# Kernel tuning notes

Hardware: AMD Instinct MI355X
Metric: run time of the kernel (lower is better)

The kernel has to match this reference:

```python
import jax, jax.numpy as jnp
import numpy as np

C_IN = 512
C = 64        # per-head dim
N_HEAD = 8
B, S = 2, 2048


def setup_inputs() -> dict:
    key = jax.random.key(0)
    ks = jax.random.split(key, 9)
    scale = 1.0 / np.sqrt(C_IN)
    return {
        "x": jax.random.normal(ks[0], (B, S, C_IN), dtype=jnp.float32),
        "bias": jax.random.normal(ks[1], (B, N_HEAD, S, S), dtype=jnp.float32),
        "Wq": jax.random.normal(ks[2], (N_HEAD * C, C_IN), dtype=jnp.float32) * scale,
        "Wk": jax.random.normal(ks[3], (N_HEAD * C, C_IN), dtype=jnp.float32) * scale,
        "Wv": jax.random.normal(ks[4], (N_HEAD * C, C_IN), dtype=jnp.float32) * scale,
        "Wo": jax.random.normal(ks[5], (C_IN, N_HEAD * C), dtype=jnp.float32) * scale,
        "bo": jax.random.normal(ks[6], (C_IN,), dtype=jnp.float32) * 0.01,
        "Wg": jax.random.normal(ks[7], (N_HEAD * C, C_IN), dtype=jnp.float32) * scale,
        "bg": jax.random.normal(ks[8], (N_HEAD * C,), dtype=jnp.float32) * 0.01,
    }


def reference(x, bias, Wq, Wk, Wv, Wo, bo, Wg, bg):
    # x: [B, S, C_IN]; attn_dim=1 -> q/k/v axis is already at -2 after movedim.
    # Project and split heads: [B, S, H*C] -> [B, H, S, C]
    def split_heads(t):
        Bq, Sq, _ = t.shape
        return t.reshape(Bq, Sq, N_HEAD, C).transpose(0, 2, 1, 3)

    q = split_heads(x @ Wq.T) / jnp.sqrt(jnp.asarray(C, x.dtype))
    k = split_heads(x @ Wk.T)
    v = split_heads(x @ Wv.T)

    a = jnp.einsum("bhqc,bhkc->bhqk", q, k) + bias   # [B, H, S, S]
    a = jax.nn.softmax(a, axis=-1)
    o = jnp.einsum("bhqk,bhkc->bhqc", a, v)          # [B, H, S, C]

    # merge heads back: [B, S, H*C]
    o = o.transpose(0, 2, 1, 3).reshape(x.shape[0], x.shape[1], N_HEAD * C)
    g = jax.nn.sigmoid(x @ Wg.T + bg)
    o = g * o
    return o @ Wo.T + bo                              # [B, S, C_IN]
```

## Files before the change

kernel.cpp:

```cpp
#include <hip/hip_runtime.h>
#include <math.h>

#define BB 2
#define HH 8
#define SS 2048
#define CC 64
#define CIN 512
#define DDIM 512
#define MM (BB*SS)
#define NCHUNK (SS / 64)

#define LOG2E 1.4426950408889634f
#define SHIFT2 (16.0f * LOG2E)

using short8  = __attribute__((ext_vector_type(8))) short;
using float4v = __attribute__((ext_vector_type(4))) float;

__device__ __forceinline__ unsigned short tob(float f) {
    unsigned u = __float_as_uint(f);
    unsigned r = (u + 0x7fffu + ((u >> 16) & 1u)) >> 16;
    return (unsigned short)r;
}
__device__ __forceinline__ float fromb(unsigned short u) {
    return __uint_as_float(((unsigned)u) << 16);
}

__device__ __forceinline__ void barrier_lds_only() {
    __builtin_amdgcn_sched_barrier(0);
    asm volatile("s_waitcnt lgkmcnt(0)" ::: "memory");
    __builtin_amdgcn_s_barrier();
    __builtin_amdgcn_sched_barrier(0);
}

__global__ __launch_bounds__(256) void convert_all(
    const float* __restrict__ x,
    const float* __restrict__ wq, const float* __restrict__ wk,
    const float* __restrict__ wv, const float* __restrict__ wg,
    const float* __restrict__ wo,
    unsigned short* __restrict__ xb,
    unsigned short* __restrict__ wqb, unsigned short* __restrict__ wkb,
    unsigned short* __restrict__ wvb, unsigned short* __restrict__ wgb,
    unsigned short* __restrict__ wob)
{
    const int NX4 = MM * CIN / 4;
    int i = blockIdx.x * blockDim.x + threadIdx.x;
    const float* src; unsigned short* dst; float scale = 1.0f; int off;
    if (i < NX4) { src = x; dst = xb; off = i; }
    else {
        int j = i - NX4;
        int seg = j >> 16;
        off = j & 65535;
        if      (seg == 0) { src = wq; dst = wqb; scale = 0.125f * LOG2E; }
        else if (seg == 1) { src = wk; dst = wkb; }
        else if (seg == 2) { src = wv; dst = wvb; }
        else if (seg == 3) { src = wg; dst = wgb; }
        else               { src = wo; dst = wob; }
    }
    float4 v = ((const float4*)src)[off];
    ushort4 o;
    o.x = tob(v.x * scale); o.y = tob(v.y * scale);
    o.z = tob(v.z * scale); o.w = tob(v.w * scale);
    ((ushort4*)dst)[off] = o;
}

__global__ __launch_bounds__(256) void proj_gemm(
    const unsigned short* __restrict__ X,
    const unsigned short* __restrict__ Wq,
    const unsigned short* __restrict__ Wk,
    const unsigned short* __restrict__ Wv,
    const unsigned short* __restrict__ Wg,
    const float* __restrict__ bg,
    unsigned short* __restrict__ Qd,
    unsigned short* __restrict__ Kd,
    unsigned short* __restrict__ Vd,
    unsigned short* __restrict__ Gd)
{
    __shared__ __align__(16) unsigned short At[64][72];
    __shared__ __align__(16) unsigned short Bt[64][72];

    int mode = blockIdx.z;
    const unsigned short* W = (mode == 0) ? Wq : (mode == 1) ? Wk : (mode == 2) ? Wv : Wg;

    int m0 = blockIdx.y * 64;
    int n0 = blockIdx.x * 64;
    int tid = threadIdx.x;
    int w = tid >> 6, lane = tid & 63;
    int quad = lane >> 4, l16 = lane & 15;
    int wm = w & 1, wn = w >> 1;

    float4v acc[2][2];
    for (int a = 0; a < 2; ++a) for (int c = 0; c < 2; ++c) acc[a][c] = (float4v)0.0f;

    for (int kc = 0; kc < CIN; kc += 64) {
        for (int it = 0; it < 2; ++it) {
            int idx = it * 2048 + tid * 8;
            int row = idx >> 6, col = idx & 63;
            *(short8*)&At[row][col] = *(const short8*)&X[(size_t)(m0 + row) * CIN + kc + col];
            *(short8*)&Bt[row][col] = *(const short8*)&W[(size_t)(n0 + row) * CIN + kc + col];
        }
        __syncthreads();
        for (int ks = 0; ks < 2; ++ks) {
            short8 a0 = *(const short8*)&At[wm * 32 + l16][ks * 32 + quad * 8];
            short8 a1 = *(const short8*)&At[wm * 32 + 16 + l16][ks * 32 + quad * 8];
            short8 b0 = *(const short8*)&Bt[wn * 32 + l16][ks * 32 + quad * 8];
            short8 b1 = *(const short8*)&Bt[wn * 32 + 16 + l16][ks * 32 + quad * 8];
            acc[0][0] = __builtin_amdgcn_mfma_f32_16x16x32_bf16(a0, b0, acc[0][0], 0, 0, 0);
            acc[0][1] = __builtin_amdgcn_mfma_f32_16x16x32_bf16(a0, b1, acc[0][1], 0, 0, 0);
            acc[1][0] = __builtin_amdgcn_mfma_f32_16x16x32_bf16(a1, b0, acc[1][0], 0, 0, 0);
            acc[1][1] = __builtin_amdgcn_mfma_f32_16x16x32_bf16(a1, b1, acc[1][1], 0, 0, 0);
        }
        __syncthreads();
    }

    if (mode == 2) {
        for (int a = 0; a < 2; ++a) for (int c = 0; c < 2; ++c)
            for (int r = 0; r < 4; ++r) {
                int ml = wm * 32 + a * 16 + quad * 4 + r;
                int nl = wn * 32 + c * 16 + l16;
                At[nl][ml] = tob(acc[a][c][r]);
            }
        __syncthreads();
        int bi = m0 >> 11, h = n0 >> 6, s0 = m0 & 2047;
        int crow = tid >> 2, seg = tid & 3;
        unsigned short* dp = Vd + (((size_t)(bi * HH + h) * CC) + crow) * SS + s0 + seg * 16;
        *(short8*)dp       = *(const short8*)&At[crow][seg * 16];
        *(short8*)(dp + 8) = *(const short8*)&At[crow][seg * 16 + 8];
        return;
    }

    for (int a = 0; a < 2; ++a) for (int c = 0; c < 2; ++c)
        for (int r = 0; r < 4; ++r) {
            int gm = m0 + wm * 32 + a * 16 + quad * 4 + r;
            int gn = n0 + wn * 32 + c * 16 + l16;
            float v = acc[a][c][r];
            if (mode <= 1) {
                int bi = gm >> 11, s = gm & 2047, h = gn >> 6, cc = gn & 63;
                unsigned short* d = (mode == 0) ? Qd : Kd;
                d[(((size_t)(bi * HH + h) * SS) + s) * CC + cc] = tob(v);
            } else {
                float g = 1.0f / (1.0f + __expf(-(v + bg[gn])));
                Gd[(size_t)gm * DDIM + gn] = tob(g);
            }
        }
}

__global__ __launch_bounds__(256, 2) void attn_kernel(
    const unsigned short* __restrict__ Q,
    const unsigned short* __restrict__ K,
    const unsigned short* __restrict__ V,
    const float* __restrict__ bias,
    const unsigned short* __restrict__ G,
    unsigned short* __restrict__ Om)
{
    __shared__ __align__(16) unsigned short Kt[64][72];
    __shared__ __align__(16) unsigned short Vt[64][72];
    __shared__ __align__(16) unsigned short Pt[4][16][72];
    __shared__ __align__(16) float Bs[64][68];

    int qb = blockIdx.x * 64;
    int bh = blockIdx.y;
    int b = bh >> 3, h = bh & 7;
    int tid = threadIdx.x;
    int w = tid >> 6, lane = tid & 63;
    int quad = lane >> 4, l16 = lane & 15;

    int phase = (blockIdx.x + blockIdx.y) & (NCHUNK - 1);

    const unsigned short* Qbh = Q + (size_t)bh * SS * CC;
    const unsigned short* Kbh = K + (size_t)bh * SS * CC;
    const unsigned short* Vbh = V + (size_t)bh * CC * SS;
    const float* Bbh = bias + (size_t)bh * SS * SS;

    int qrow = qb + w * 16 + l16;
    short8 aq0 = *(const short8*)&Qbh[(size_t)qrow * CC + quad * 8];
    short8 aq1 = *(const short8*)&Qbh[(size_t)qrow * CC + 32 + quad * 8];

    float lsum[4] = {0.f, 0.f, 0.f, 0.f};
    float4v accO[4];
    for (int jn = 0; jn < 4; ++jn) accO[jn] = (float4v)0.0f;

    int srow0 = (tid * 8) >> 6,        scol0 = (tid * 8) & 63;
    int srow1 = (2048 + tid * 8) >> 6, scol1 = (2048 + tid * 8) & 63;
    int btrow = tid >> 4;
    int btcol = (tid & 15) * 4;

    short8 pk0, pk1, pv0, pv1;
    float4 pb[4];
    {
        int kb0 = phase * 64;
        pk0 = *(const short8*)&Kbh[(size_t)(kb0 + srow0) * CC + scol0];
        pk1 = *(const short8*)&Kbh[(size_t)(kb0 + srow1) * CC + scol1];
        pv0 = *(const short8*)&Vbh[(size_t)srow0 * SS + kb0 + scol0];
        pv1 = *(const short8*)&Vbh[(size_t)srow1 * SS + kb0 + scol1];
#pragma unroll
        for (int rr = 0; rr < 4; ++rr)
            pb[rr] = *(const float4*)&Bbh[(size_t)(qb + rr * 16 + btrow) * SS + kb0 + btcol];
    }

    for (int c = 0; c < NCHUNK; ++c) {
        barrier_lds_only();
        *(short8*)&Kt[srow0][scol0] = pk0;
        *(short8*)&Kt[srow1][scol1] = pk1;
        *(short8*)&Vt[srow0][scol0] = pv0;
        *(short8*)&Vt[srow1][scol1] = pv1;
#pragma unroll
        for (int rr = 0; rr < 4; ++rr)
            *(float4*)&Bs[rr * 16 + btrow][btcol] = pb[rr];

        if (c + 1 < NCHUNK) {
            int kbn = ((c + 1 + phase) & (NCHUNK - 1)) * 64;
            pk0 = *(const short8*)&Kbh[(size_t)(kbn + srow0) * CC + scol0];
            pk1 = *(const short8*)&Kbh[(size_t)(kbn + srow1) * CC + scol1];
            pv0 = *(const short8*)&Vbh[(size_t)srow0 * SS + kbn + scol0];
            pv1 = *(const short8*)&Vbh[(size_t)srow1 * SS + kbn + scol1];
#pragma unroll
            for (int rr = 0; rr < 4; ++rr)
                pb[rr] = *(const float4*)&Bbh[(size_t)(qb + rr * 16 + btrow) * SS + kbn + btcol];
        }

        barrier_lds_only();

        float4v sa[4];
#pragma unroll
        for (int j = 0; j < 4; ++j) sa[j] = (float4v)(-SHIFT2);
#pragma unroll
        for (int j = 0; j < 4; ++j) {
            short8 bk0 = *(const short8*)&Kt[j * 16 + l16][quad * 8];
            short8 bk1 = *(const short8*)&Kt[j * 16 + l16][32 + quad * 8];
            sa[j] = __builtin_amdgcn_mfma_f32_16x16x32_bf16(aq0, bk0, sa[j], 0, 0, 0);
            sa[j] = __builtin_amdgcn_mfma_f32_16x16x32_bf16(aq1, bk1, sa[j], 0, 0, 0);
        }

#pragma unroll
        for (int j = 0; j < 4; ++j)
#pragma unroll
            for (int r = 0; r < 4; ++r) {
                float bb = Bs[w * 16 + quad * 4 + r][j * 16 + l16];
                float p = __builtin_amdgcn_exp2f(fmaf(bb, LOG2E, sa[j][r]));
                lsum[r] += p;
                Pt[w][quad * 4 + r][j * 16 + l16] = tob(p);
            }

#pragma unroll
        for (int ks = 0; ks < 2; ++ks) {
            short8 ap = *(const short8*)&Pt[w][l16][ks * 32 + quad * 8];
#pragma unroll
            for (int jn = 0; jn < 4; ++jn) {
                short8 bv = *(const short8*)&Vt[jn * 16 + l16][ks * 32 + quad * 8];
                accO[jn] = __builtin_amdgcn_mfma_f32_16x16x32_bf16(ap, bv, accO[jn], 0, 0, 0);
            }
        }
    }

    float rl[4];
#pragma unroll
    for (int r = 0; r < 4; ++r) {
        float s = lsum[r];
        s += __shfl_xor(s, 1, 64);
        s += __shfl_xor(s, 2, 64);
        s += __shfl_xor(s, 4, 64);
        s += __shfl_xor(s, 8, 64);
        rl[r] = 1.0f / s;
    }

    int mrow = b * SS + qb + w * 16 + quad * 4;
#pragma unroll
    for (int jn = 0; jn < 4; ++jn)
#pragma unroll
        for (int r = 0; r < 4; ++r) {
            int col = h * 64 + jn * 16 + l16;
            float g = fromb(G[(size_t)(mrow + r) * DDIM + col]);
            Om[(size_t)(mrow + r) * DDIM + col] = tob(accO[jn][r] * rl[r] * g);
        }
}

__global__ __launch_bounds__(256) void out_gemm(
    const unsigned short* __restrict__ Og,
    const unsigned short* __restrict__ W,
    const float* __restrict__ bo,
    float* __restrict__ out)
{
    __shared__ __align__(16) unsigned short At[64][72];
    __shared__ __align__(16) unsigned short Bt[64][72];

    int m0 = blockIdx.y * 64;
    int n0 = blockIdx.x * 64;
    int tid = threadIdx.x;
    int w = tid >> 6, lane = tid & 63;
    int quad = lane >> 4, l16 = lane & 15;
    int wm = w & 1, wn = w >> 1;

    float4v acc[2][2];
    for (int a = 0; a < 2; ++a) for (int c = 0; c < 2; ++c) acc[a][c] = (float4v)0.0f;

    for (int kc = 0; kc < DDIM; kc += 64) {
        for (int it = 0; it < 2; ++it) {
            int idx = it * 2048 + tid * 8;
            int row = idx >> 6, col = idx & 63;
            *(short8*)&At[row][col] = *(const short8*)&Og[(size_t)(m0 + row) * DDIM + kc + col];
            *(short8*)&Bt[row][col] = *(const short8*)&W[(size_t)(n0 + row) * DDIM + kc + col];
        }
        __syncthreads();
        for (int ks = 0; ks < 2; ++ks) {
            short8 a0 = *(const short8*)&At[wm * 32 + l16][ks * 32 + quad * 8];
            short8 a1 = *(const short8*)&At[wm * 32 + 16 + l16][ks * 32 + quad * 8];
            short8 b0 = *(const short8*)&Bt[wn * 32 + l16][ks * 32 + quad * 8];
            short8 b1 = *(const short8*)&Bt[wn * 32 + 16 + l16][ks * 32 + quad * 8];
            acc[0][0] = __builtin_amdgcn_mfma_f32_16x16x32_bf16(a0, b0, acc[0][0], 0, 0, 0);
            acc[0][1] = __builtin_amdgcn_mfma_f32_16x16x32_bf16(a0, b1, acc[0][1], 0, 0, 0);
            acc[1][0] = __builtin_amdgcn_mfma_f32_16x16x32_bf16(a1, b0, acc[1][0], 0, 0, 0);
            acc[1][1] = __builtin_amdgcn_mfma_f32_16x16x32_bf16(a1, b1, acc[1][1], 0, 0, 0);
        }
        __syncthreads();
    }

    for (int a = 0; a < 2; ++a) for (int c = 0; c < 2; ++c)
        for (int r = 0; r < 4; ++r) {
            int gm = m0 + wm * 32 + a * 16 + quad * 4 + r;
            int gn = n0 + wn * 32 + c * 16 + l16;
            out[(size_t)gm * DDIM + gn] = acc[a][c][r] + bo[gn];
        }
}

extern "C" void kernel_launch(void* const* d_in, const int* in_sizes, int n_in,
                              void* d_out, int out_size, void* d_ws, size_t ws_size,
                              hipStream_t stream)
{
    const float* x    = (const float*)d_in[0];
    const float* bias = (const float*)d_in[1];
    const float* Wq   = (const float*)d_in[2];
    const float* Wk   = (const float*)d_in[3];
    const float* Wv   = (const float*)d_in[4];
    const float* Wo   = (const float*)d_in[5];
    const float* bo   = (const float*)d_in[6];
    const float* Wg   = (const float*)d_in[7];
    const float* bg   = (const float*)d_in[8];
    float* out = (float*)d_out;

    char* ws = (char*)d_ws;
    auto alloc = [&](size_t bytes) { char* p = ws; ws += (bytes + 255) & ~(size_t)255; return p; };
    unsigned short* xb  = (unsigned short*)alloc((size_t)MM * CIN * 2);
    unsigned short* wqb = (unsigned short*)alloc((size_t)DDIM * CIN * 2);
    unsigned short* wkb = (unsigned short*)alloc((size_t)DDIM * CIN * 2);
    unsigned short* wvb = (unsigned short*)alloc((size_t)DDIM * CIN * 2);
    unsigned short* wgb = (unsigned short*)alloc((size_t)DDIM * CIN * 2);
    unsigned short* wob = (unsigned short*)alloc((size_t)DDIM * CIN * 2);
    unsigned short* Qh  = (unsigned short*)alloc((size_t)BB * HH * SS * CC * 2);
    unsigned short* Kh  = (unsigned short*)alloc((size_t)BB * HH * SS * CC * 2);
    unsigned short* Vh  = (unsigned short*)alloc((size_t)BB * HH * SS * CC * 2);
    unsigned short* Gt  = (unsigned short*)alloc((size_t)MM * DDIM * 2);
    unsigned short* Om  = (unsigned short*)alloc((size_t)MM * DDIM * 2);

    convert_all<<<3328, 256, 0, stream>>>(x, Wq, Wk, Wv, Wg, Wo,
                                          xb, wqb, wkb, wvb, wgb, wob);
    proj_gemm<<<dim3(DDIM / 64, MM / 64, 4), 256, 0, stream>>>(
        xb, wqb, wkb, wvb, wgb, bg, Qh, Kh, Vh, Gt);
    attn_kernel<<<dim3(SS / 64, BB * HH), 256, 0, stream>>>(
        Qh, Kh, Vh, bias, Gt, Om);
    out_gemm<<<dim3(DDIM / 64, MM / 64), 256, 0, stream>>>(Om, wob, bo, out);
}
```

Before: 493.0 us.

## Stage K/V/bias tiles via direct global-to-LDS loads with double buffering

Replaces register-staged prefetch of K, V and bias tiles with global_load_lds transfers straight into double-buffered LDS, issuing the load two chunks ahead and synchronizing with vmcnt waits. K and V tiles drop the row padding and use an XOR swizzle on 16-byte columns to avoid bank conflicts. The aim is to free VGPRs, remove the LDS store instructions and overlap memory traffic with compute. The cost is more LDS (the bias buffer doubles), which may limit occupancy, and fragile hand-written waitcnt counts.

```diff
diff --git a/kernel.cpp b/kernel.cpp
--- a/kernel.cpp
+++ b/kernel.cpp
@@ -25,12 +25,10 @@
     return __uint_as_float(((unsigned)u) << 16);
 }
 
-__device__ __forceinline__ void barrier_lds_only() {
-    __builtin_amdgcn_sched_barrier(0);
-    asm volatile("s_waitcnt lgkmcnt(0)" ::: "memory");
-    __builtin_amdgcn_s_barrier();
-    __builtin_amdgcn_sched_barrier(0);
-}
+#define GLDS(srcp, ldsp)                                                     \
+    __builtin_amdgcn_global_load_lds(                                        \
+        (const __attribute__((address_space(1))) void*)(srcp),               \
+        (__attribute__((address_space(3))) void*)(ldsp), 16, 0, 0)
 
 __global__ __launch_bounds__(256) void convert_all(
     const float* __restrict__ x,
@@ -152,10 +150,10 @@
     const unsigned short* __restrict__ G,
     unsigned short* __restrict__ Om)
 {
-    __shared__ __align__(16) unsigned short Kt[64][72];
-    __shared__ __align__(16) unsigned short Vt[64][72];
+    __shared__ __align__(16) unsigned short Kt[2][64][64];
+    __shared__ __align__(16) unsigned short Vt[2][64][64];
+    __shared__ __align__(16) float Bs[2][64][64];
     __shared__ __align__(16) unsigned short Pt[4][16][72];
-    __shared__ __align__(16) float Bs[64][68];
 
     int qb = blockIdx.x * 64;
     int bh = blockIdx.y;
@@ -163,6 +161,7 @@
     int tid = threadIdx.x;
     int w = tid >> 6, lane = tid & 63;
     int quad = lane >> 4, l16 = lane & 15;
+    int swl = l16 & 7;
 
     int phase = (blockIdx.x + blockIdx.y) & (NCHUNK - 1);
 
@@ -179,54 +178,46 @@
     float4v accO[4];
     for (int jn = 0; jn < 4; ++jn) accO[jn] = (float4v)0.0f;
 
-    int srow0 = (tid * 8) >> 6,        scol0 = (tid * 8) & 63;
-    int srow1 = (2048 + tid * 8) >> 6, scol1 = (2048 + tid * 8) & 63;
-    int btrow = tid >> 4;
-    int btcol = (tid & 15) * 4;
-
-    short8 pk0, pk1, pv0, pv1;
-    float4 pb[4];
-    {
-        int kb0 = phase * 64;
-        pk0 = *(const short8*)&Kbh[(size_t)(kb0 + srow0) * CC + scol0];
-        pk1 = *(const short8*)&Kbh[(size_t)(kb0 + srow1) * CC + scol1];
-        pv0 = *(const short8*)&Vbh[(size_t)srow0 * SS + kb0 + scol0];
-        pv1 = *(const short8*)&Vbh[(size_t)srow1 * SS + kb0 + scol1];
-#pragma unroll
-        for (int rr = 0; rr < 4; ++rr)
-            pb[rr] = *(const float4*)&Bbh[(size_t)(qb + rr * 16 + btrow) * SS + kb0 + btcol];
-    }
+    int row8  = lane >> 3;
+    int kswz  = (lane & 7) ^ row8;
+    int row16 = lane >> 4;
+    int col16 = lane & 15;
+
+    auto STAGE = [&](int d, int kb) {
+#pragma unroll
+        for (int p = 0; p < 2; ++p) {
+            int r0 = w * 16 + p * 8;
+            GLDS(Kbh + (size_t)(kb + r0 + row8) * CC + kswz * 8, &Kt[d][r0][0]);
+            GLDS(Vbh + (size_t)(r0 + row8) * SS + kb + kswz * 8, &Vt[d][r0][0]);
+        }
+#pragma unroll
+        for (int t = 0; t < 4; ++t) {
+            int r0 = w * 16 + t * 4;
+            GLDS(Bbh + (size_t)(qb + r0 + row16) * SS + kb + col16 * 4, &Bs[d][r0][0]);
+        }
+    };
+
+    STAGE(0, phase * 64);
+    STAGE(1, ((1 + phase) & (NCHUNK - 1)) * 64);
 
     for (int c = 0; c < NCHUNK; ++c) {
-        barrier_lds_only();
-        *(short8*)&Kt[srow0][scol0] = pk0;
-        *(short8*)&Kt[srow1][scol1] = pk1;
-        *(short8*)&Vt[srow0][scol0] = pv0;
-        *(short8*)&Vt[srow1][scol1] = pv1;
-#pragma unroll
-        for (int rr = 0; rr < 4; ++rr)
-            *(float4*)&Bs[rr * 16 + btrow][btcol] = pb[rr];
-
+        int d = c & 1;
         if (c + 1 < NCHUNK) {
-            int kbn = ((c + 1 + phase) & (NCHUNK - 1)) * 64;
-            pk0 = *(const short8*)&Kbh[(size_t)(kbn + srow0) * CC + scol0];
-            pk1 = *(const short8*)&Kbh[(size_t)(kbn + srow1) * CC + scol1];
-            pv0 = *(const short8*)&Vbh[(size_t)srow0 * SS + kbn + scol0];
-            pv1 = *(const short8*)&Vbh[(size_t)srow1 * SS + kbn + scol1];
-#pragma unroll
-            for (int rr = 0; rr < 4; ++rr)
-                pb[rr] = *(const float4*)&Bbh[(size_t)(qb + rr * 16 + btrow) * SS + kbn + btcol];
-        }
-
-        barrier_lds_only();
+            asm volatile("s_waitcnt vmcnt(8)" ::: "memory");
+        } else {
+            asm volatile("s_waitcnt vmcnt(0)" ::: "memory");
+        }
+        __builtin_amdgcn_sched_barrier(0);
+        __builtin_amdgcn_s_barrier();
+        __builtin_amdgcn_sched_barrier(0);
 
         float4v sa[4];
 #pragma unroll
         for (int j = 0; j < 4; ++j) sa[j] = (float4v)(-SHIFT2);
 #pragma unroll
         for (int j = 0; j < 4; ++j) {
-            short8 bk0 = *(const short8*)&Kt[j * 16 + l16][quad * 8];
-            short8 bk1 = *(const short8*)&Kt[j * 16 + l16][32 + quad * 8];
+            short8 bk0 = *(const short8*)&Kt[d][j * 16 + l16][((quad    ) ^ swl) * 8];
+            short8 bk1 = *(const short8*)&Kt[d][j * 16 + l16][((quad + 4) ^ swl) * 8];
             sa[j] = __builtin_amdgcn_mfma_f32_16x16x32_bf16(aq0, bk0, sa[j], 0, 0, 0);
             sa[j] = __builtin_amdgcn_mfma_f32_16x16x32_bf16(aq1, bk1, sa[j], 0, 0, 0);
         }
@@ -235,7 +226,7 @@
         for (int j = 0; j < 4; ++j)
 #pragma unroll
             for (int r = 0; r < 4; ++r) {
-                float bb = Bs[w * 16 + quad * 4 + r][j * 16 + l16];
+                float bb = Bs[d][w * 16 + quad * 4 + r][j * 16 + l16];
                 float p = __builtin_amdgcn_exp2f(fmaf(bb, LOG2E, sa[j][r]));
                 lsum[r] += p;
                 Pt[w][quad * 4 + r][j * 16 + l16] = tob(p);
@@ -246,10 +237,18 @@
             short8 ap = *(const short8*)&Pt[w][l16][ks * 32 + quad * 8];
 #pragma unroll
             for (int jn = 0; jn < 4; ++jn) {
-                short8 bv = *(const short8*)&Vt[jn * 16 + l16][ks * 32 + quad * 8];
+                short8 bv = *(const short8*)&Vt[d][jn * 16 + l16][((ks * 4 + quad) ^ swl) * 8];
                 accO[jn] = __builtin_amdgcn_mfma_f32_16x16x32_bf16(ap, bv, accO[jn], 0, 0, 0);
             }
         }
+
+        __builtin_amdgcn_sched_barrier(0);
+        asm volatile("s_waitcnt lgkmcnt(0)" ::: "memory");
+        __builtin_amdgcn_s_barrier();
+        __builtin_amdgcn_sched_barrier(0);
+
+        if (c + 2 < NCHUNK)
+            STAGE(d, ((c + 2 + phase) & (NCHUNK - 1)) * 64);
     }
 
     float rl[4];
```

Measured after the change: 450.1 us. 1.1x faster.
